# Optimization experiments

Hardware: AMD Instinct MI355X
Metric: run time of the kernel (lower is better)

Reference implementation:

```python
import jax, jax.numpy as jnp
import numpy as np

B, S, D, H, L = 16, 1024, 128, 8, 3
DFF = 4 * D  # 512
DH = D // H  # 16
NUM_CLASSES = 6


def layernorm(x, g, b, eps):
    mu = jnp.mean(x, axis=-1, keepdims=True)
    var = jnp.mean(jnp.square(x - mu), axis=-1, keepdims=True)
    return g * (x - mu) / jnp.sqrt(var + eps) + b


def setup_inputs() -> dict:
    key = jax.random.key(0)
    ks = jax.random.split(key, 16)
    sc = 0.05
    inp = {
        'x': jax.random.normal(ks[0], (B, S, D), dtype=jnp.float32),
        'Wq': jax.random.normal(ks[1], (L, D, D), dtype=jnp.float32) * sc,
        'bq': jnp.zeros((L, D), dtype=jnp.float32),
        'Wk': jax.random.normal(ks[2], (L, D, D), dtype=jnp.float32) * sc,
        'bk': jnp.zeros((L, D), dtype=jnp.float32),
        'Wv': jax.random.normal(ks[3], (L, D, D), dtype=jnp.float32) * sc,
        'bv': jnp.zeros((L, D), dtype=jnp.float32),
        'ln1_g': jnp.ones((L, D), dtype=jnp.float32),
        'ln1_b': jnp.zeros((L, D), dtype=jnp.float32),
        'W1': jax.random.normal(ks[4], (L, D, DFF), dtype=jnp.float32) * sc,
        'b1': jnp.zeros((L, DFF), dtype=jnp.float32),
        'W2': jax.random.normal(ks[5], (L, DFF, D), dtype=jnp.float32) * sc,
        'b2': jnp.zeros((L, D), dtype=jnp.float32),
        'ln2_g': jnp.ones((L, D), dtype=jnp.float32),
        'ln2_b': jnp.zeros((L, D), dtype=jnp.float32),
        'Wout': jax.random.normal(ks[6], (D, NUM_CLASSES), dtype=jnp.float32) * sc,
        'bout': jnp.zeros((NUM_CLASSES,), dtype=jnp.float32),
    }
    return inp


def reference(x, Wq, bq, Wk, bk, Wv, bv, ln1_g, ln1_b, W1, b1, W2, b2, ln2_g, ln2_b, Wout, bout):
    scale = 1.0 / jnp.sqrt(jnp.float32(DH))
    for l in range(L):
        # Q/K/V projections with ReLU activation (as in source Dense(..., relu))
        q = jax.nn.relu(jnp.einsum('bsd,de->bse', x, Wq[l]) + bq[l])
        k = jax.nn.relu(jnp.einsum('bsd,de->bse', x, Wk[l]) + bk[l])
        v = jax.nn.relu(jnp.einsum('bsd,de->bse', x, Wv[l]) + bv[l])
        # split-heads (tf.split axis=-1 / concat axis=0 == reshape to heads)
        qh = q.reshape(B, S, H, DH)
        kh = k.reshape(B, S, H, DH)
        vh = v.reshape(B, S, H, DH)
        scores = jnp.einsum('bqhd,bkhd->bhqk', qh, kh) * scale  # [B,H,S,S]
        attn = jax.nn.softmax(scores, axis=-1)
        o = jnp.einsum('bhqk,bkhd->bqhd', attn, vh).reshape(B, S, D)
        x = layernorm(o + x, ln1_g[l], ln1_b[l], 1e-8)
        # pointwise FFN (Conv1D kernel_size=1 == dense over last dim)
        h = jax.nn.relu(jnp.einsum('bsd,df->bsf', x, W1[l]) + b1[l])
        f = jnp.einsum('bsf,fd->bsd', h, W2[l]) + b2[l]
        x = layernorm(f + x, ln2_g[l], ln2_b[l], 1e-6)
    return jnp.einsum('bsd,dc->bsc', x, Wout) + bout
```

## Files before the change

### kernel.cpp

```cpp
#include <hip/hip_runtime.h>
#include <math.h>

#define Bq 16
#define Sq 1024
#define Dq 128
#define Hq 8
#define DHq 16
#define DFFq 512
#define Lq 3
#define NCLS 6
#define NROWS (Bq * Sq)
#define NX ((size_t)NROWS * Dq)

#define QSCL 0.36067376022224085f

typedef __attribute__((ext_vector_type(8))) short    bf16x8;
typedef __attribute__((ext_vector_type(4))) float    f32x4;
typedef __attribute__((ext_vector_type(4))) _Float16 f16x4;
typedef __attribute__((ext_vector_type(8))) _Float16 f16x8;
typedef __attribute__((ext_vector_type(2))) _Float16 f16x2;

__device__ inline ushort f32_to_bf16(float f) {
    union { float f; unsigned u; } v; v.f = f;
    unsigned r = v.u + 0x7fffu + ((v.u >> 16) & 1u);
    return (ushort)(r >> 16);
}

__device__ __forceinline__ float exp2_raw(float x) {
    float r;
    asm("v_exp_f32 %0, %1" : "=v"(r) : "v"(x));
    return r;
}

__device__ __forceinline__ float rcp_fast(float x) {
    float r;
    asm("v_rcp_f32 %0, %1" : "=v"(r) : "v"(x));
    return r;
}

__device__ __forceinline__ f16x2 pkrtz(float a, float b) {
    return __builtin_bit_cast(f16x2, __builtin_amdgcn_cvt_pkrtz(a, b));
}

__global__ __launch_bounds__(256) void prep_kernel(
    const float* __restrict__ Wqp, const float* __restrict__ Wkp,
    const float* __restrict__ Wvp, const float* __restrict__ W1p,
    const float* __restrict__ W2p, const float* __restrict__ xp,
    ushort* __restrict__ wbf, ushort* __restrict__ xbf)
{
    const int gid = blockIdx.x * 256 + threadIdx.x;
    if (gid < 147456) {
        const int w   = gid / 49152;
        const int rem = gid - w * 49152;
        const int l   = rem >> 14;
        const int idx = rem & 16383;
        const int k   = idx >> 7;
        const int n   = idx & 127;
        const float* src = (w == 0) ? Wqp : (w == 1) ? Wkp : Wvp;
        const float scl = (w == 0) ? QSCL : 1.0f;
        wbf[(size_t)(w * 3 + l) * 16384 + n * 128 + k] =
            f32_to_bf16(src[(size_t)l * 16384 + k * 128 + n] * scl);
    } else if (gid < 344064) {
        const int g   = gid - 147456;
        const int l   = g >> 16;
        const int idx = g & 65535;
        const int k   = idx >> 9;
        const int n   = idx & 511;
        wbf[147456 + (size_t)l * 65536 + n * 128 + k] =
            f32_to_bf16(W1p[(size_t)l * 65536 + k * 512 + n]);
    } else if (gid < 540672) {
        const int g   = gid - 344064;
        const int l   = g >> 16;
        const int idx = g & 65535;
        const int k   = idx >> 7;
        const int n   = idx & 127;
        wbf[344064 + (size_t)l * 65536 + n * 512 + k] =
            f32_to_bf16(W2p[(size_t)l * 65536 + k * 128 + n]);
    } else {
        const int g = gid - 540672;
        xbf[g] = f32_to_bf16(xp[g]);
    }
}

__global__ __launch_bounds__(256) void gemm_qkv(
    const ushort* __restrict__ A,
    const ushort* __restrict__ wq, const ushort* __restrict__ wk,
    const ushort* __restrict__ wv,
    const float* __restrict__ bqp, const float* __restrict__ bkp,
    const float* __restrict__ bvp,
    _Float16* __restrict__ qo, _Float16* __restrict__ ko,
    _Float16* __restrict__ vo)
{
    __shared__ ushort As[64 * 40];
    __shared__ ushort Bs[128 * 40];

    const int sel  = blockIdx.y;
    const ushort* Bt   = (sel == 0) ? wq : (sel == 1) ? wk : wv;
    const float*  bias = (sel == 0) ? bqp : (sel == 1) ? bkp : bvp;
    const float   bscl = (sel == 0) ? QSCL : 1.0f;

    const int tid  = threadIdx.x;
    const int row0 = blockIdx.x * 64;
    const int wave = tid >> 6;
    const int lane = tid & 63;
    const int quad = lane >> 4;
    const int m16  = lane & 15;
    const int wm   = wave >> 1;
    const int wn   = wave & 1;

    const int sar = tid >> 2;
    const int sac = (tid & 3) * 8;

    f32x4 acc[2][4];
    #pragma unroll
    for (int i = 0; i < 2; ++i)
        #pragma unroll
        for (int j = 0; j < 4; ++j) acc[i][j] = (f32x4)0.f;

    const int r1 = tid >> 2, r2 = r1 + 64;

    bf16x8 av  = *(const bf16x8*)(A  + (size_t)(row0 + sar) * 128 + sac);
    bf16x8 bv1 = *(const bf16x8*)(Bt + (size_t)r1 * 128 + sac);
    bf16x8 bv2 = *(const bf16x8*)(Bt + (size_t)r2 * 128 + sac);

    for (int k0 = 0; k0 < 128; k0 += 32) {
        __syncthreads();
        *(bf16x8*)&As[sar * 40 + sac] = av;
        *(bf16x8*)&Bs[r1 * 40 + sac]  = bv1;
        *(bf16x8*)&Bs[r2 * 40 + sac]  = bv2;
        __syncthreads();

        if (k0 < 96) {
            av  = *(const bf16x8*)(A  + (size_t)(row0 + sar) * 128 + k0 + 32 + sac);
            bv1 = *(const bf16x8*)(Bt + (size_t)r1 * 128 + k0 + 32 + sac);
            bv2 = *(const bf16x8*)(Bt + (size_t)r2 * 128 + k0 + 32 + sac);
        }

        bf16x8 af[2], bf[4];
        #pragma unroll
        for (int i = 0; i < 2; ++i)
            af[i] = *(const bf16x8*)&As[(32 * wm + 16 * i + m16) * 40 + quad * 8];
        #pragma unroll
        for (int j = 0; j < 4; ++j)
            bf[j] = *(const bf16x8*)&Bs[(64 * wn + 16 * j + m16) * 40 + quad * 8];
        #pragma unroll
        for (int i = 0; i < 2; ++i)
            #pragma unroll
            for (int j = 0; j < 4; ++j)
                acc[i][j] = __builtin_amdgcn_mfma_f32_16x16x32_bf16(af[i], bf[j], acc[i][j], 0, 0, 0);
    }

    #pragma unroll
    for (int i = 0; i < 2; ++i) {
        #pragma unroll
        for (int j = 0; j < 4; ++j) {
            const int col = 64 * wn + 16 * j + m16;
            const float bb = bias[col] * bscl;
            const int hh = col >> 4, dh = col & 15;
            #pragma unroll
            for (int r = 0; r < 4; ++r) {
                float val = fmaxf(acc[i][j][r] + bb, 0.f);
                const int gr = row0 + 32 * wm + 16 * i + quad * 4 + r;
                const int b = gr >> 10, s = gr & 1023;
                if (sel == 2) {
                    vo[(((size_t)b * Hq + hh) * DHq + dh) * Sq + s] = (_Float16)val;
                } else {
                    _Float16* outp = (sel == 0) ? qo : ko;
                    outp[(((size_t)b * Hq + hh) * Sq + s) * DHq + dh] = (_Float16)val;
                }
            }
        }
    }
}

__global__ __launch_bounds__(256) void gemm_ffn_fused(
    const _Float16* __restrict__ o, const float* __restrict__ resid,
    const float* __restrict__ g1, const float* __restrict__ beta1,
    const ushort* __restrict__ W1t, const float* __restrict__ bias1,
    const ushort* __restrict__ W2t, const float* __restrict__ bias2,
    const float* __restrict__ g2, const float* __restrict__ beta2,
    float* __restrict__ xb,
    const ushort* __restrict__ wqn, const ushort* __restrict__ wkn,
    const ushort* __restrict__ wvn,
    const float* __restrict__ bqn, const float* __restrict__ bkn,
    const float* __restrict__ bvn,
    _Float16* __restrict__ qo, _Float16* __restrict__ ko,
    _Float16* __restrict__ vo, int do_next,
    const float* __restrict__ Wout, const float* __restrict__ bout,
    float* __restrict__ out, int last)
{
    __shared__ __align__(16) char smem[69120];
    ushort*    Af   = (ushort*)smem;
    ushort*    Hs   = (ushort*)(smem + 8704);
    ushort*    Bs   = (ushort*)(smem + 41984);
    float*     wo_s = (float*)(smem + 41984);
    _Float16*  vals = (_Float16*)(smem + 60416);
    float*     mus  = (float*)(smem + 68864);
    float*     rsds = (float*)(smem + 68992);

    const int tid  = threadIdx.x;
    const int row0 = blockIdx.x * 32;
    const int wave = tid >> 6;
    const int lane = tid & 63;
    const int quad = lane >> 4;
    const int m16  = lane & 15;
    const int wm   = wave >> 1;
    const int wn   = wave & 1;
    const int sac  = (tid & 3) * 8;
    const int r1   = tid >> 2, r2 = r1 + 64;

    const int ca = lane * 2;
    const float2 gg  = *(const float2*)(g1 + ca);
    const float2 bt1 = *(const float2*)(beta1 + ca);
    #pragma unroll 2
    for (int it = 0; it < 8; ++it) {
        const int rr = wave * 8 + it;
        const size_t base = (size_t)(row0 + rr) * Dq;
        const f16x2  ov = *(const f16x2*)(o + base + ca);
        const float2 rv = *(const float2*)(resid + base + ca);
        const float v0 = (float)ov[0] + rv.x;
        const float v1 = (float)ov[1] + rv.y;

        float s = v0 + v1;
        #pragma unroll
        for (int off = 32; off > 0; off >>= 1) s += __shfl_xor(s, off, 64);
        const float mu = s * (1.f / 128.f);
        const float d0 = v0 - mu, d1 = v1 - mu;
        float vs = d0 * d0 + d1 * d1;
        #pragma unroll
        for (int off = 32; off > 0; off >>= 1) vs += __shfl_xor(vs, off, 64);
        const float rstd = rsqrtf(vs * (1.f / 128.f) + 1e-8f);

        const float rv0 = gg.x * d0 * rstd + bt1.x;
        const float rv1 = gg.y * d1 * rstd + bt1.y;
        ushort2 ab; ab.x = f32_to_bf16(rv0); ab.y = f32_to_bf16(rv1);
        *(ushort2*)&Af[rr * 136 + ca] = ab;
        f16x2 vv; vv[0] = (_Float16)rv0; vv[1] = (_Float16)rv1;
        *(f16x2*)&vals[rr * 132 + ca] = vv;
    }

    f32x4 acc[4];
    #pragma unroll
    for (int j = 0; j < 4; ++j) acc[j] = (f32x4)0.f;

    bf16x8 w11 = *(const bf16x8*)(W1t + (size_t)r1 * 128 + sac);
    bf16x8 w12 = *(const bf16x8*)(W1t + (size_t)r1 * 128 + 32 + sac);
    bf16x8 w21 = *(const bf16x8*)(W1t + (size_t)r2 * 128 + sac);
    bf16x8 w22 = *(const bf16x8*)(W1t + (size_t)r2 * 128 + 32 + sac);

    for (int idx = 0; idx < 8; ++idx) {
        const int cc = idx >> 1;
        const int k0 = (idx & 1) * 64;

        __syncthreads();
        *(bf16x8*)&Bs[r1 * 72 + sac]      = w11;
        *(bf16x8*)&Bs[r1 * 72 + 32 + sac] = w12;
        *(bf16x8*)&Bs[r2 * 72 + sac]      = w21;
        *(bf16x8*)&Bs[r2 * 72 + 32 + sac] = w22;
        __syncthreads();

        if (idx < 7) {
            const int cc2 = (idx + 1) >> 1;
            const int k02 = ((idx + 1) & 1) * 64;
            w11 = *(const bf16x8*)(W1t + (size_t)(cc2 * 128 + r1) * 128 + k02 + sac);
            w12 = *(const bf16x8*)(W1t + (size_t)(cc2 * 128 + r1) * 128 + k02 + 32 + sac);
            w21 = *(const bf16x8*)(W1t + (size_t)(cc2 * 128 + r2) * 128 + k02 + sac);
            w22 = *(const bf16x8*)(W1t + (size_t)(cc2 * 128 + r2) * 128 + k02 + 32 + sac);
        }

        #pragma unroll
        for (int hh = 0; hh < 2; ++hh) {
            const int kk = k0 + hh * 32;
            const bf16x8 af = *(const bf16x8*)&Af[(16 * wm + m16) * 136 + kk + quad * 8];
            bf16x8 bf[4];
            #pragma unroll
            for (int j = 0; j < 4; ++j)
                bf[j] = *(const bf16x8*)&Bs[(64 * wn + 16 * j + m16) * 72 + hh * 32 + quad * 8];
            #pragma unroll
            for (int j = 0; j < 4; ++j)
                acc[j] = __builtin_amdgcn_mfma_f32_16x16x32_bf16(af, bf[j], acc[j], 0, 0, 0);
        }

        if (idx & 1) {
            #pragma unroll
            for (int j = 0; j < 4; ++j) {
                const int col = cc * 128 + 64 * wn + 16 * j + m16;
                const float bb = bias1[col];
                #pragma unroll
                for (int r = 0; r < 4; ++r) {
                    const int row = 16 * wm + quad * 4 + r;
                    Hs[row * 520 + col] = f32_to_bf16(fmaxf(acc[j][r] + bb, 0.f));
                }
                acc[j] = (f32x4)0.f;
            }
        }
    }

    f32x4 acc2[4];
    #pragma unroll
    for (int j = 0; j < 4; ++j) acc2[j] = (f32x4)0.f;

    w11 = *(const bf16x8*)(W2t + (size_t)r1 * DFFq + sac);
    w12 = *(const bf16x8*)(W2t + (size_t)r1 * DFFq + 32 + sac);
    w21 = *(const bf16x8*)(W2t + (size_t)r2 * DFFq + sac);
    w22 = *(const bf16x8*)(W2t + (size_t)r2 * DFFq + 32 + sac);

    for (int kc = 0; kc < 8; ++kc) {
        const int k0 = kc * 64;

        __syncthreads();
        *(bf16x8*)&Bs[r1 * 72 + sac]      = w11;
        *(bf16x8*)&Bs[r1 * 72 + 32 + sac] = w12;
        *(bf16x8*)&Bs[r2 * 72 + sac]      = w21;
        *(bf16x8*)&Bs[r2 * 72 + 32 + sac] = w22;
        __syncthreads();

        if (kc < 7) {
            const int k02 = (kc + 1) * 64;
            w11 = *(const bf16x8*)(W2t + (size_t)r1 * DFFq + k02 + sac);
            w12 = *(const bf16x8*)(W2t + (size_t)r1 * DFFq + k02 + 32 + sac);
            w21 = *(const bf16x8*)(W2t + (size_t)r2 * DFFq + k02 + sac);
            w22 = *(const bf16x8*)(W2t + (size_t)r2 * DFFq + k02 + 32 + sac);
        }

        #pragma unroll
        for (int hh = 0; hh < 2; ++hh) {
            const int kk = k0 + hh * 32;
            const bf16x8 af = *(const bf16x8*)&Hs[(16 * wm + m16) * 520 + kk + quad * 8];
            bf16x8 bf[4];
            #pragma unroll
            for (int j = 0; j < 4; ++j)
                bf[j] = *(const bf16x8*)&Bs[(64 * wn + 16 * j + m16) * 72 + hh * 32 + quad * 8];
            #pragma unroll
            for (int j = 0; j < 4; ++j)
                acc2[j] = __builtin_amdgcn_mfma_f32_16x16x32_bf16(af, bf[j], acc2[j], 0, 0, 0);
        }
    }

    __syncthreads();

    float vreg[4][4];
    #pragma unroll
    for (int j = 0; j < 4; ++j) {
        const int col = 64 * wn + 16 * j + m16;
        const float bb = bias2[col];
        #pragma unroll
        for (int r = 0; r < 4; ++r) {
            const int row = 16 * wm + quad * 4 + r;
            float v = acc2[j][r] + bb + (float)vals[row * 132 + col];
            vreg[j][r] = v;
            vals[row * 132 + col] = (_Float16)v;
        }
    }
    if (last) {
        #pragma unroll
        for (int i = 0; i < 3; ++i) wo_s[tid + i * 256] = Wout[tid + i * 256];
    }
    __syncthreads();

    {
        const int row = tid >> 3;
        const int c0  = (tid & 7) * 16;
        float s = 0.f, s2 = 0.f;
        #pragma unroll
        for (int u = 0; u < 4; ++u) {
            const f16x4 xv = *(const f16x4*)&vals[row * 132 + c0 + u * 4];
            #pragma unroll
            for (int e = 0; e < 4; ++e) {
                const float x = (float)xv[e];
                s += x; s2 = fmaf(x, x, s2);
            }
        }
        s  += __shfl_xor(s, 1, 64);  s  += __shfl_xor(s, 2, 64);  s  += __shfl_xor(s, 4, 64);
        s2 += __shfl_xor(s2, 1, 64); s2 += __shfl_xor(s2, 2, 64); s2 += __shfl_xor(s2, 4, 64);
        if ((tid & 7) == 0) {
            const float mu  = s * (1.f / 128.f);
            const float var = s2 * (1.f / 128.f) - mu * mu;
            mus[row]  = mu;
            rsds[row] = rsqrtf(var + 1e-6f);
        }
    }
    __syncthreads();

    if (!last) {
        #pragma unroll
        for (int j = 0; j < 4; ++j) {
            const int col = 64 * wn + 16 * j + m16;
            #pragma unroll
            for (int r = 0; r < 4; ++r) {
                const int row = 16 * wm + quad * 4 + r;
                const float rn = g2[col] * (vreg[j][r] - mus[row]) * rsds[row] + beta2[col];
                xb[(size_t)(row0 + row) * Dq + col] = rn;
                Af[row * 136 + col] = f32_to_bf16(rn);
            }
        }

        if (do_next) {
            bf16x8 q11 = *(const bf16x8*)(wqn + (size_t)r1 * 128 + sac);
            bf16x8 q12 = *(const bf16x8*)(wqn + (size_t)r1 * 128 + 32 + sac);
            bf16x8 q21 = *(const bf16x8*)(wqn + (size_t)r2 * 128 + sac);
            bf16x8 q22 = *(const bf16x8*)(wqn + (size_t)r2 * 128 + 32 + sac);

            f32x4 qacc[4];
            for (int st = 0; st < 6; ++st) {
                const int sel  = st >> 1;
                const int half = st & 1;
                if (half == 0) {
                    #pragma unroll
                    for (int j = 0; j < 4; ++j) qacc[j] = (f32x4)0.f;
                }

                __syncthreads();
                *(bf16x8*)&Bs[r1 * 72 + sac]      = q11;
                *(bf16x8*)&Bs[r1 * 72 + 32 + sac] = q12;
                *(bf16x8*)&Bs[r2 * 72 + sac]      = q21;
                *(bf16x8*)&Bs[r2 * 72 + 32 + sac] = q22;
                __syncthreads();

                if (st < 5) {
                    const int sel2 = (st + 1) >> 1;
                    const int k02  = ((st + 1) & 1) * 64;
                    const ushort* Bt2 = (sel2 == 0) ? wqn : (sel2 == 1) ? wkn : wvn;
                    q11 = *(const bf16x8*)(Bt2 + (size_t)r1 * 128 + k02 + sac);
                    q12 = *(const bf16x8*)(Bt2 + (size_t)r1 * 128 + k02 + 32 + sac);
                    q21 = *(const bf16x8*)(Bt2 + (size_t)r2 * 128 + k02 + sac);
                    q22 = *(const bf16x8*)(Bt2 + (size_t)r2 * 128 + k02 + 32 + sac);
                }

                const int k0 = half * 64;
                #pragma unroll
                for (int hh = 0; hh < 2; ++hh) {
                    const int kk = k0 + hh * 32;
                    const bf16x8 af = *(const bf16x8*)&Af[(16 * wm + m16) * 136 + kk + quad * 8];
                    bf16x8 bf[4];
                    #pragma unroll
                    for (int j = 0; j < 4; ++j)
                        bf[j] = *(const bf16x8*)&Bs[(64 * wn + 16 * j + m16) * 72 + hh * 32 + quad * 8];
                    #pragma unroll
                    for (int j = 0; j < 4; ++j)
                        qacc[j] = __builtin_amdgcn_mfma_f32_16x16x32_bf16(af, bf[j], qacc[j], 0, 0, 0);
                }

                if (half) {
                    const float* bias = (sel == 0) ? bqn : (sel == 1) ? bkn : bvn;
                    const float  bscl = (sel == 0) ? QSCL : 1.0f;
                    #pragma unroll
                    for (int j = 0; j < 4; ++j) {
                        const int col = 64 * wn + 16 * j + m16;
                        const float bb = bias[col] * bscl;
                        const int hh = col >> 4, dh = col & 15;
                        #pragma unroll
                        for (int r = 0; r < 4; ++r) {
                            float val = fmaxf(qacc[j][r] + bb, 0.f);
                            const int gr = row0 + 16 * wm + quad * 4 + r;
                            const int b = gr >> 10, s = gr & 1023;
                            if (sel == 2) {
                                vo[(((size_t)b * Hq + hh) * DHq + dh) * Sq + s] = (_Float16)val;
                            } else {
                                _Float16* outp = (sel == 0) ? qo : ko;
                                outp[(((size_t)b * Hq + hh) * Sq + s) * DHq + dh] = (_Float16)val;
                            }
                        }
                    }
                }
            }
        }
    } else {
        #pragma unroll
        for (int j = 0; j < 4; ++j) {
            const int col = 64 * wn + 16 * j + m16;
            #pragma unroll
            for (int r = 0; r < 4; ++r) {
                const int row = 16 * wm + quad * 4 + r;
                vals[row * 132 + col] =
                    (_Float16)(g2[col] * (vreg[j][r] - mus[row]) * rsds[row] + beta2[col]);
            }
        }
        __syncthreads();
        if (tid < 32 * NCLS) {
            const int row = tid / NCLS;
            const int c   = tid - row * NCLS;
            float a = bout[c];
            #pragma unroll 8
            for (int kk = 0; kk < Dq; ++kk)
                a = fmaf((float)vals[row * 132 + kk], wo_s[kk * NCLS + c], a);
            out[(size_t)(row0 + row) * NCLS + c] = a;
        }
    }
}

__global__ __launch_bounds__(256) void attn_mfma(
    const _Float16* __restrict__ q, const _Float16* __restrict__ k,
    const _Float16* __restrict__ vt, _Float16* __restrict__ o)
{
    __shared__ _Float16 Ks[256 * 20];
    __shared__ _Float16 Vs[16 * 264];

    const int bh   = blockIdx.x;
    const int qc   = blockIdx.y;
    const int b    = bh >> 3;
    const int h    = bh & 7;
    const int tid  = threadIdx.x;
    const int wave = tid >> 6;
    const int lane = tid & 63;
    const int quad = lane >> 4;
    const int m16  = lane & 15;
    const int q0   = qc * 128 + wave * 32;

    const f16x4 qf0 = *(const f16x4*)(q + (((size_t)bh * Sq) + q0 + m16) * DHq + quad * 4);
    const f16x4 qf1 = *(const f16x4*)(q + (((size_t)bh * Sq) + q0 + 16 + m16) * DHq + quad * 4);

    const _Float16* kg  = k  + (size_t)bh * Sq * DHq;
    const _Float16* vtg = vt + (size_t)bh * DHq * Sq;

    f32x4 oacc0 = (f32x4)0.f, oacc1 = (f32x4)0.f;
    float lacc0 = 0.f, lacc1 = 0.f;

    const int krow = tid;
    const int vrow = tid >> 4;
    const int vcol = (tid & 15) * 16;

    f16x8 ka  = *(const f16x8*)(kg + (size_t)krow * DHq);
    f16x8 kb8 = *(const f16x8*)(kg + (size_t)krow * DHq + 8);
    f16x8 va  = *(const f16x8*)(vtg + (size_t)vrow * Sq + vcol);
    f16x8 vb  = *(const f16x8*)(vtg + (size_t)vrow * Sq + vcol + 8);

    for (int kb = 0; kb < 4; ++kb) {
        __syncthreads();
        *(f16x8*)&Ks[krow * 20 + 0] = ka;
        *(f16x8*)&Ks[krow * 20 + 8] = kb8;
        *(f16x8*)&Vs[vrow * 264 + vcol + 0] = va;
        *(f16x8*)&Vs[vrow * 264 + vcol + 8] = vb;
        __syncthreads();

        if (kb < 3) {
            const _Float16* kp = kg  + ((size_t)(kb + 1) * 256 + krow) * DHq;
            const _Float16* vp = vtg + (size_t)vrow * Sq + (kb + 1) * 256 + vcol;
            ka  = *(const f16x8*)(kp);
            kb8 = *(const f16x8*)(kp + 8);
            va  = *(const f16x8*)(vp);
            vb  = *(const f16x8*)(vp + 8);
        }

        #pragma unroll 4
        for (int kt = 0; kt < 16; ++kt) {
            const f16x4 kf = *(const f16x4*)&Ks[(kt * 16 + m16) * 20 + quad * 4];
            const f16x4 vf = *(const f16x4*)&Vs[m16 * 264 + kt * 16 + quad * 4];

            f32x4 st0 = __builtin_amdgcn_mfma_f32_16x16x16f16(kf, qf0, (f32x4)0.f, 0, 0, 0);
            f32x4 st1 = __builtin_amdgcn_mfma_f32_16x16x16f16(kf, qf1, (f32x4)0.f, 0, 0, 0);

            const float p00 = exp2_raw(st0[0]);
            const float p01 = exp2_raw(st0[1]);
            const float p02 = exp2_raw(st0[2]);
            const float p03 = exp2_raw(st0[3]);
            const float p10 = exp2_raw(st1[0]);
            const float p11 = exp2_raw(st1[1]);
            const float p12 = exp2_raw(st1[2]);
            const float p13 = exp2_raw(st1[3]);

            lacc0 += (p00 + p01) + (p02 + p03);
            lacc1 += (p10 + p11) + (p12 + p13);

            const f16x2 a0 = pkrtz(p00, p01);
            const f16x2 a1 = pkrtz(p02, p03);
            const f16x2 b0 = pkrtz(p10, p11);
            const f16x2 b1 = pkrtz(p12, p13);

            const f16x4 pf0 = __builtin_shufflevector(a0, a1, 0, 1, 2, 3);
            const f16x4 pf1 = __builtin_shufflevector(b0, b1, 0, 1, 2, 3);

            oacc0 = __builtin_amdgcn_mfma_f32_16x16x16f16(pf0, vf, oacc0, 0, 0, 0);
            oacc1 = __builtin_amdgcn_mfma_f32_16x16x16f16(pf1, vf, oacc1, 0, 0, 0);
        }
    }

    lacc0 += __shfl_xor(lacc0, 16, 64);
    lacc0 += __shfl_xor(lacc0, 32, 64);
    lacc1 += __shfl_xor(lacc1, 16, 64);
    lacc1 += __shfl_xor(lacc1, 32, 64);

    const float linv0 = rcp_fast(lacc0);
    const float linv1 = rcp_fast(lacc1);

    #pragma unroll
    for (int r = 0; r < 4; ++r) {
        const float i0 = __shfl(linv0, quad * 4 + r, 64);
        const float i1 = __shfl(linv1, quad * 4 + r, 64);
        o[((size_t)b * Sq + q0 + quad * 4 + r) * Dq + h * DHq + m16]      = (_Float16)(oacc0[r] * i0);
        o[((size_t)b * Sq + q0 + 16 + quad * 4 + r) * Dq + h * DHq + m16] = (_Float16)(oacc1[r] * i1);
    }
}

extern "C" void kernel_launch(void* const* d_in, const int* in_sizes, int n_in,
                              void* d_out, int out_size, void* d_ws, size_t ws_size,
                              hipStream_t stream)
{
    const float* x_in  = (const float*)d_in[0];
    const float* Wq    = (const float*)d_in[1];
    const float* bq    = (const float*)d_in[2];
    const float* Wk    = (const float*)d_in[3];
    const float* bk    = (const float*)d_in[4];
    const float* Wv    = (const float*)d_in[5];
    const float* bv    = (const float*)d_in[6];
    const float* ln1_g = (const float*)d_in[7];
    const float* ln1_b = (const float*)d_in[8];
    const float* W1    = (const float*)d_in[9];
    const float* b1    = (const float*)d_in[10];
    const float* W2    = (const float*)d_in[11];
    const float* b2    = (const float*)d_in[12];
    const float* ln2_g = (const float*)d_in[13];
    const float* ln2_b = (const float*)d_in[14];
    const float* Wout  = (const float*)d_in[15];
    const float* bout  = (const float*)d_in[16];
    float* out = (float*)d_out;

    float* ws = (float*)d_ws;
    _Float16* qf16 = (_Float16*)ws;
    _Float16* kf16 = (_Float16*)(ws + NX / 2);
    _Float16* vt16 = (_Float16*)(ws + NX);
    float*    xb   = ws + 9 * NX / 2;
    ushort*   xbf0 = (ushort*)(ws + 11 * NX / 2);
    ushort*   wbf  = (ushort*)(ws + 7 * NX);
    _Float16* obuf = (_Float16*)(ws + 8 * NX);

    prep_kernel<<<dim3(10304), dim3(256), 0, stream>>>(Wq, Wk, Wv, W1, W2, x_in, wbf, xbf0);

    const dim3 blk(256);

    {
        const ushort* wqt = wbf + (size_t)0 * 16384;
        const ushort* wkt = wbf + (size_t)3 * 16384;
        const ushort* wvt = wbf + (size_t)6 * 16384;
        gemm_qkv<<<dim3(256, 3), blk, 0, stream>>>(
            xbf0, wqt, wkt, wvt, bq, bk, bv, qf16, kf16, vt16);
    }

    const float* xcur = x_in;
    for (int l = 0; l < Lq; ++l) {
        const ushort* w1t = wbf + 147456 + (size_t)l * 65536;
        const ushort* w2t = wbf + 344064 + (size_t)l * 65536;
        const int next = (l < Lq - 1) ? 1 : 0;
        const int ln   = l + 1;
        const ushort* wqn = next ? (wbf + (size_t)(0 * 3 + ln) * 16384) : wbf;
        const ushort* wkn = next ? (wbf + (size_t)(1 * 3 + ln) * 16384) : wbf;
        const ushort* wvn = next ? (wbf + (size_t)(2 * 3 + ln) * 16384) : wbf;
        const float*  bqn = next ? (bq + ln * Dq) : bq;
        const float*  bkn = next ? (bk + ln * Dq) : bk;
        const float*  bvn = next ? (bv + ln * Dq) : bv;

        attn_mfma<<<dim3(Bq * Hq, 8), blk, 0, stream>>>(qf16, kf16, vt16, obuf);

        gemm_ffn_fused<<<dim3(512), blk, 0, stream>>>(
            obuf, xcur, ln1_g + l * Dq, ln1_b + l * Dq,
            w1t, b1 + l * DFFq, w2t, b2 + l * Dq,
            ln2_g + l * Dq, ln2_b + l * Dq,
            xb,
            wqn, wkn, wvn, bqn, bkn, bvn,
            qf16, kf16, vt16, next,
            Wout, bout, out, (l == Lq - 1) ? 1 : 0);

        xcur = xb;
    }
}
```

Before: 248.5 us.

## Read GEMM weights directly from global, shrink LDS, compute softmax denominators via MFMA

The QKV GEMM now stages the full A tile in LDS once and reads weight fragments straight from global memory, removing per-k-step barriers. The fused FFN kernel does the same for W1, W2 and the next-layer QKV weights, drops the B-tile LDS buffer so shared memory shrinks, and adds a launch_bounds occupancy hint of 3 blocks. In attention, the softmax row sums are accumulated with an extra MFMA against a ones vector instead of scalar adds and cross-lane shuffles. The risks are uncoalesced global weight loads that lean on cache instead of LDS reuse, the extra MFMA work, and register pressure from the occupancy hint.

```diff
diff --git a/kernel.cpp b/kernel.cpp
--- a/kernel.cpp
+++ b/kernel.cpp
@@ -91,8 +91,7 @@
     _Float16* __restrict__ qo, _Float16* __restrict__ ko,
     _Float16* __restrict__ vo)
 {
-    __shared__ ushort As[64 * 40];
-    __shared__ ushort Bs[128 * 40];
+    __shared__ ushort As[64 * 136];
 
     const int sel  = blockIdx.y;
     const ushort* Bt   = (sel == 0) ? wq : (sel == 1) ? wk : wv;
@@ -108,8 +107,15 @@
     const int wm   = wave >> 1;
     const int wn   = wave & 1;
 
-    const int sar = tid >> 2;
-    const int sac = (tid & 3) * 8;
+    const int sar  = tid >> 2;
+    const int sac0 = (tid & 3) * 8;
+
+    #pragma unroll
+    for (int c = 0; c < 4; ++c) {
+        bf16x8 av = *(const bf16x8*)(A + (size_t)(row0 + sar) * 128 + c * 32 + sac0);
+        *(bf16x8*)&As[sar * 136 + c * 32 + sac0] = av;
+    }
+    __syncthreads();
 
     f32x4 acc[2][4];
     #pragma unroll
@@ -117,37 +123,20 @@
         #pragma unroll
         for (int j = 0; j < 4; ++j) acc[i][j] = (f32x4)0.f;
 
-    const int r1 = tid >> 2, r2 = r1 + 64;
-
-    bf16x8 av  = *(const bf16x8*)(A  + (size_t)(row0 + sar) * 128 + sac);
-    bf16x8 bv1 = *(const bf16x8*)(Bt + (size_t)r1 * 128 + sac);
-    bf16x8 bv2 = *(const bf16x8*)(Bt + (size_t)r2 * 128 + sac);
-
+    #pragma unroll 2
     for (int k0 = 0; k0 < 128; k0 += 32) {
-        __syncthreads();
-        *(bf16x8*)&As[sar * 40 + sac] = av;
-        *(bf16x8*)&Bs[r1 * 40 + sac]  = bv1;
-        *(bf16x8*)&Bs[r2 * 40 + sac]  = bv2;
-        __syncthreads();
-
-        if (k0 < 96) {
-            av  = *(const bf16x8*)(A  + (size_t)(row0 + sar) * 128 + k0 + 32 + sac);
-            bv1 = *(const bf16x8*)(Bt + (size_t)r1 * 128 + k0 + 32 + sac);
-            bv2 = *(const bf16x8*)(Bt + (size_t)r2 * 128 + k0 + 32 + sac);
-        }
-
-        bf16x8 af[2], bf[4];
+        bf16x8 af[2], bfv[4];
         #pragma unroll
         for (int i = 0; i < 2; ++i)
-            af[i] = *(const bf16x8*)&As[(32 * wm + 16 * i + m16) * 40 + quad * 8];
+            af[i] = *(const bf16x8*)&As[(32 * wm + 16 * i + m16) * 136 + k0 + quad * 8];
         #pragma unroll
         for (int j = 0; j < 4; ++j)
-            bf[j] = *(const bf16x8*)&Bs[(64 * wn + 16 * j + m16) * 40 + quad * 8];
+            bfv[j] = *(const bf16x8*)(Bt + (size_t)(64 * wn + 16 * j + m16) * 128 + k0 + quad * 8);
         #pragma unroll
         for (int i = 0; i < 2; ++i)
             #pragma unroll
             for (int j = 0; j < 4; ++j)
-                acc[i][j] = __builtin_amdgcn_mfma_f32_16x16x32_bf16(af[i], bf[j], acc[i][j], 0, 0, 0);
+                acc[i][j] = __builtin_amdgcn_mfma_f32_16x16x32_bf16(af[i], bfv[j], acc[i][j], 0, 0, 0);
     }
 
     #pragma unroll
@@ -173,7 +162,7 @@
     }
 }
 
-__global__ __launch_bounds__(256) void gemm_ffn_fused(
+__global__ __launch_bounds__(256, 3) void gemm_ffn_fused(
     const _Float16* __restrict__ o, const float* __restrict__ resid,
     const float* __restrict__ g1, const float* __restrict__ beta1,
     const ushort* __restrict__ W1t, const float* __restrict__ bias1,
@@ -189,14 +178,13 @@
     const float* __restrict__ Wout, const float* __restrict__ bout,
     float* __restrict__ out, int last)
 {
-    __shared__ __align__(16) char smem[69120];
+    __shared__ __align__(16) char smem[53760];
     ushort*    Af   = (ushort*)smem;
     ushort*    Hs   = (ushort*)(smem + 8704);
-    ushort*    Bs   = (ushort*)(smem + 41984);
-    float*     wo_s = (float*)(smem + 41984);
-    _Float16*  vals = (_Float16*)(smem + 60416);
-    float*     mus  = (float*)(smem + 68864);
-    float*     rsds = (float*)(smem + 68992);
+    _Float16*  vals = (_Float16*)(smem + 41984);
+    float*     wo_s = (float*)(smem + 50432);
+    float*     mus  = (float*)(smem + 53504);
+    float*     rsds = (float*)(smem + 53632);
 
     const int tid  = threadIdx.x;
     const int row0 = blockIdx.x * 32;
@@ -206,8 +194,6 @@
     const int m16  = lane & 15;
     const int wm   = wave >> 1;
     const int wn   = wave & 1;
-    const int sac  = (tid & 3) * 8;
-    const int r1   = tid >> 2, r2 = r1 + 64;
 
     const int ca = lane * 2;
     const float2 gg  = *(const float2*)(g1 + ca);
@@ -238,49 +224,28 @@
         f16x2 vv; vv[0] = (_Float16)rv0; vv[1] = (_Float16)rv1;
         *(f16x2*)&vals[rr * 132 + ca] = vv;
     }
+    __syncthreads();
 
     f32x4 acc[4];
     #pragma unroll
     for (int j = 0; j < 4; ++j) acc[j] = (f32x4)0.f;
 
-    bf16x8 w11 = *(const bf16x8*)(W1t + (size_t)r1 * 128 + sac);
-    bf16x8 w12 = *(const bf16x8*)(W1t + (size_t)r1 * 128 + 32 + sac);
-    bf16x8 w21 = *(const bf16x8*)(W1t + (size_t)r2 * 128 + sac);
-    bf16x8 w22 = *(const bf16x8*)(W1t + (size_t)r2 * 128 + 32 + sac);
-
+    #pragma unroll 2
     for (int idx = 0; idx < 8; ++idx) {
         const int cc = idx >> 1;
         const int k0 = (idx & 1) * 64;
-
-        __syncthreads();
-        *(bf16x8*)&Bs[r1 * 72 + sac]      = w11;
-        *(bf16x8*)&Bs[r1 * 72 + 32 + sac] = w12;
-        *(bf16x8*)&Bs[r2 * 72 + sac]      = w21;
-        *(bf16x8*)&Bs[r2 * 72 + 32 + sac] = w22;
-        __syncthreads();
-
-        if (idx < 7) {
-            const int cc2 = (idx + 1) >> 1;
-            const int k02 = ((idx + 1) & 1) * 64;
-            w11 = *(const bf16x8*)(W1t + (size_t)(cc2 * 128 + r1) * 128 + k02 + sac);
-            w12 = *(const bf16x8*)(W1t + (size_t)(cc2 * 128 + r1) * 128 + k02 + 32 + sac);
-            w21 = *(const bf16x8*)(W1t + (size_t)(cc2 * 128 + r2) * 128 + k02 + sac);
-            w22 = *(const bf16x8*)(W1t + (size_t)(cc2 * 128 + r2) * 128 + k02 + 32 + sac);
-        }
-
         #pragma unroll
         for (int hh = 0; hh < 2; ++hh) {
             const int kk = k0 + hh * 32;
             const bf16x8 af = *(const bf16x8*)&Af[(16 * wm + m16) * 136 + kk + quad * 8];
-            bf16x8 bf[4];
+            bf16x8 bfv[4];
             #pragma unroll
             for (int j = 0; j < 4; ++j)
-                bf[j] = *(const bf16x8*)&Bs[(64 * wn + 16 * j + m16) * 72 + hh * 32 + quad * 8];
+                bfv[j] = *(const bf16x8*)(W1t + (size_t)(cc * 128 + 64 * wn + 16 * j + m16) * 128 + kk + quad * 8);
             #pragma unroll
             for (int j = 0; j < 4; ++j)
-                acc[j] = __builtin_amdgcn_mfma_f32_16x16x32_bf16(af, bf[j], acc[j], 0, 0, 0);
-        }
-
+                acc[j] = __builtin_amdgcn_mfma_f32_16x16x32_bf16(af, bfv[j], acc[j], 0, 0, 0);
+        }
         if (idx & 1) {
             #pragma unroll
             for (int j = 0; j < 4; ++j) {
@@ -295,49 +260,28 @@
             }
         }
     }
+    __syncthreads();
 
     f32x4 acc2[4];
     #pragma unroll
     for (int j = 0; j < 4; ++j) acc2[j] = (f32x4)0.f;
 
-    w11 = *(const bf16x8*)(W2t + (size_t)r1 * DFFq + sac);
-    w12 = *(const bf16x8*)(W2t + (size_t)r1 * DFFq + 32 + sac);
-    w21 = *(const bf16x8*)(W2t + (size_t)r2 * DFFq + sac);
-    w22 = *(const bf16x8*)(W2t + (size_t)r2 * DFFq + 32 + sac);
-
+    #pragma unroll 2
     for (int kc = 0; kc < 8; ++kc) {
         const int k0 = kc * 64;
-
-        __syncthreads();
-        *(bf16x8*)&Bs[r1 * 72 + sac]      = w11;
-        *(bf16x8*)&Bs[r1 * 72 + 32 + sac] = w12;
-        *(bf16x8*)&Bs[r2 * 72 + sac]      = w21;
-        *(bf16x8*)&Bs[r2 * 72 + 32 + sac] = w22;
-        __syncthreads();
-
-        if (kc < 7) {
-            const int k02 = (kc + 1) * 64;
-            w11 = *(const bf16x8*)(W2t + (size_t)r1 * DFFq + k02 + sac);
-            w12 = *(const bf16x8*)(W2t + (size_t)r1 * DFFq + k02 + 32 + sac);
-            w21 = *(const bf16x8*)(W2t + (size_t)r2 * DFFq + k02 + sac);
-            w22 = *(const bf16x8*)(W2t + (size_t)r2 * DFFq + k02 + 32 + sac);
-        }
-
         #pragma unroll
         for (int hh = 0; hh < 2; ++hh) {
             const int kk = k0 + hh * 32;
             const bf16x8 af = *(const bf16x8*)&Hs[(16 * wm + m16) * 520 + kk + quad * 8];
-            bf16x8 bf[4];
+            bf16x8 bfv[4];
             #pragma unroll
             for (int j = 0; j < 4; ++j)
-                bf[j] = *(const bf16x8*)&Bs[(64 * wn + 16 * j + m16) * 72 + hh * 32 + quad * 8];
+                bfv[j] = *(const bf16x8*)(W2t + (size_t)(64 * wn + 16 * j + m16) * DFFq + kk + quad * 8);
             #pragma unroll
             for (int j = 0; j < 4; ++j)
-                acc2[j] = __builtin_amdgcn_mfma_f32_16x16x32_bf16(af, bf[j], acc2[j], 0, 0, 0);
-        }
-    }
-
-    __syncthreads();
+                acc2[j] = __builtin_amdgcn_mfma_f32_16x16x32_bf16(af, bfv[j], acc2[j], 0, 0, 0);
+        }
+    }
 
     float vreg[4][4];
     #pragma unroll
@@ -394,51 +338,31 @@
                 Af[row * 136 + col] = f32_to_bf16(rn);
             }
         }
+        __syncthreads();
 
         if (do_next) {
-            bf16x8 q11 = *(const bf16x8*)(wqn + (size_t)r1 * 128 + sac);
-            bf16x8 q12 = *(const bf16x8*)(wqn + (size_t)r1 * 128 + 32 + sac);
-            bf16x8 q21 = *(const bf16x8*)(wqn + (size_t)r2 * 128 + sac);
-            bf16x8 q22 = *(const bf16x8*)(wqn + (size_t)r2 * 128 + 32 + sac);
-
             f32x4 qacc[4];
+            #pragma unroll 2
             for (int st = 0; st < 6; ++st) {
                 const int sel  = st >> 1;
                 const int half = st & 1;
+                const ushort* Bt2 = (sel == 0) ? wqn : (sel == 1) ? wkn : wvn;
                 if (half == 0) {
                     #pragma unroll
                     for (int j = 0; j < 4; ++j) qacc[j] = (f32x4)0.f;
                 }
-
-                __syncthreads();
-                *(bf16x8*)&Bs[r1 * 72 + sac]      = q11;
-                *(bf16x8*)&Bs[r1 * 72 + 32 + sac] = q12;
-                *(bf16x8*)&Bs[r2 * 72 + sac]      = q21;
-                *(bf16x8*)&Bs[r2 * 72 + 32 + sac] = q22;
-                __syncthreads();
-
-                if (st < 5) {
-                    const int sel2 = (st + 1) >> 1;
-                    const int k02  = ((st + 1) & 1) * 64;
-                    const ushort* Bt2 = (sel2 == 0) ? wqn : (sel2 == 1) ? wkn : wvn;
-                    q11 = *(const bf16x8*)(Bt2 + (size_t)r1 * 128 + k02 + sac);
-                    q12 = *(const bf16x8*)(Bt2 + (size_t)r1 * 128 + k02 + 32 + sac);
-                    q21 = *(const bf16x8*)(Bt2 + (size_t)r2 * 128 + k02 + sac);
-                    q22 = *(const bf16x8*)(Bt2 + (size_t)r2 * 128 + k02 + 32 + sac);
-                }
-
                 const int k0 = half * 64;
                 #pragma unroll
                 for (int hh = 0; hh < 2; ++hh) {
                     const int kk = k0 + hh * 32;
                     const bf16x8 af = *(const bf16x8*)&Af[(16 * wm + m16) * 136 + kk + quad * 8];
-                    bf16x8 bf[4];
+                    bf16x8 bfv[4];
                     #pragma unroll
                     for (int j = 0; j < 4; ++j)
-                        bf[j] = *(const bf16x8*)&Bs[(64 * wn + 16 * j + m16) * 72 + hh * 32 + quad * 8];
+                        bfv[j] = *(const bf16x8*)(Bt2 + (size_t)(64 * wn + 16 * j + m16) * 128 + kk + quad * 8);
                     #pragma unroll
                     for (int j = 0; j < 4; ++j)
-                        qacc[j] = __builtin_amdgcn_mfma_f32_16x16x32_bf16(af, bf[j], qacc[j], 0, 0, 0);
+                        qacc[j] = __builtin_amdgcn_mfma_f32_16x16x32_bf16(af, bfv[j], qacc[j], 0, 0, 0);
                 }
 
                 if (half) {
@@ -514,7 +438,11 @@
     const _Float16* vtg = vt + (size_t)bh * DHq * Sq;
 
     f32x4 oacc0 = (f32x4)0.f, oacc1 = (f32x4)0.f;
-    float lacc0 = 0.f, lacc1 = 0.f;
+    f32x4 dacc0 = (f32x4)0.f, dacc1 = (f32x4)0.f;
+
+    f16x4 onesf;
+    onesf[0] = (_Float16)1.f; onesf[1] = (_Float16)1.f;
+    onesf[2] = (_Float16)1.f; onesf[3] = (_Float16)1.f;
 
     const int krow = tid;
     const int vrow = tid >> 4;
@@ -550,43 +478,25 @@
             f32x4 st0 = __builtin_amdgcn_mfma_f32_16x16x16f16(kf, qf0, (f32x4)0.f, 0, 0, 0);
             f32x4 st1 = __builtin_amdgcn_mfma_f32_16x16x16f16(kf, qf1, (f32x4)0.f, 0, 0, 0);
 
-            const float p00 = exp2_raw(st0[0]);
-            const float p01 = exp2_raw(st0[1]);
-            const float p02 = exp2_raw(st0[2]);
-            const float p03 = exp2_raw(st0[3]);
-            const float p10 = exp2_raw(st1[0]);
-            const float p11 = exp2_raw(st1[1]);
-            const float p12 = exp2_raw(st1[2]);
-            const float p13 = exp2_raw(st1[3]);
-
-            lacc0 += (p00 + p01) + (p02 + p03);
-            lacc1 += (p10 + p11) + (p12 + p13);
-
-            const f16x2 a0 = pkrtz(p00, p01);
-            const f16x2 a1 = pkrtz(p02, p03);
-            const f16x2 b0 = pkrtz(p10, p11);
-            const f16x2 b1 = pkrtz(p12, p13);
+            const f16x2 a0 = pkrtz(exp2_raw(st0[0]), exp2_raw(st0[1]));
+            const f16x2 a1 = pkrtz(exp2_raw(st0[2]), exp2_raw(st0[3]));
+            const f16x2 b0 = pkrtz(exp2_raw(st1[0]), exp2_raw(st1[1]));
+            const f16x2 b1 = pkrtz(exp2_raw(st1[2]), exp2_raw(st1[3]));
 
             const f16x4 pf0 = __builtin_shufflevector(a0, a1, 0, 1, 2, 3);
             const f16x4 pf1 = __builtin_shufflevector(b0, b1, 0, 1, 2, 3);
 
             oacc0 = __builtin_amdgcn_mfma_f32_16x16x16f16(pf0, vf, oacc0, 0, 0, 0);
             oacc1 = __builtin_amdgcn_mfma_f32_16x16x16f16(pf1, vf, oacc1, 0, 0, 0);
-        }
-    }
-
-    lacc0 += __shfl_xor(lacc0, 16, 64);
-    lacc0 += __shfl_xor(lacc0, 32, 64);
-    lacc1 += __shfl_xor(lacc1, 16, 64);
-    lacc1 += __shfl_xor(lacc1, 32, 64);
-
-    const float linv0 = rcp_fast(lacc0);
-    const float linv1 = rcp_fast(lacc1);
+            dacc0 = __builtin_amdgcn_mfma_f32_16x16x16f16(pf0, onesf, dacc0, 0, 0, 0);
+            dacc1 = __builtin_amdgcn_mfma_f32_16x16x16f16(pf1, onesf, dacc1, 0, 0, 0);
+        }
+    }
 
     #pragma unroll
     for (int r = 0; r < 4; ++r) {
-        const float i0 = __shfl(linv0, quad * 4 + r, 64);
-        const float i1 = __shfl(linv1, quad * 4 + r, 64);
+        const float i0 = rcp_fast(dacc0[r]);
+        const float i1 = rcp_fast(dacc1[r]);
         o[((size_t)b * Sq + q0 + quad * 4 + r) * Dq + h * DHq + m16]      = (_Float16)(oacc0[r] * i0);
         o[((size_t)b * Sq + q0 + 16 + quad * 4 + r) * Dq + h * DHq + m16] = (_Float16)(oacc1[r] * i1);
     }
```

Result: slower. 318.8 us (+28.3%).
